# Optimization experiments

Hardware: AMD Instinct MI355X
Metric: run time of the kernel (lower is better)

Reference implementation:

```python
import jax, jax.numpy as jnp
import numpy as np

IN_FEATURES = 4096
TOKENS = 8192


def setup_inputs() -> dict:
    key = jax.random.key(0)
    k1, k2, k3 = jax.random.split(key, 3)
    x = jax.random.normal(k1, (TOKENS, IN_FEATURES), dtype=jnp.float32)
    # original init: uniform(-1, 1)
    weight = jax.random.uniform(k2, (IN_FEATURES,), dtype=jnp.float32, minval=-1.0, maxval=1.0)
    bias = jax.random.uniform(k3, (IN_FEATURES,), dtype=jnp.float32, minval=-1.0, maxval=1.0)
    return {"x": x, "weight": weight, "bias": bias}


def reference(x, weight, bias):
    # F.linear(x, eye(n) * w) + b == x * w + b (elementwise over last dim)
    return x * weight + bias
```

## Files before the change

### kernel.cpp

```cpp
#include <hip/hip_runtime.h>


#define IN_FEATURES 4096
#define VEC 4
#define WVECS (IN_FEATURES / VEC)

__global__ __launch_bounds__(256) void one_to_one_kernel(
        const float4* __restrict__ x,
        const float4* __restrict__ w,
        const float4* __restrict__ b,
        float4* __restrict__ out,
        int nvec) {
    int i = blockIdx.x * blockDim.x + threadIdx.x;
    if (i >= nvec) return;

    int col = i & (WVECS - 1);

    float4 xv = x[i];
    float4 wv = w[col];
    float4 bv = b[col];
    float4 ov;
    ov.x = fmaf(xv.x, wv.x, bv.x);
    ov.y = fmaf(xv.y, wv.y, bv.y);
    ov.z = fmaf(xv.z, wv.z, bv.z);
    ov.w = fmaf(xv.w, wv.w, bv.w);
    out[i] = ov;
}

extern "C" void kernel_launch(void* const* d_in, const int* in_sizes, int n_in,
                              void* d_out, int out_size, void* d_ws, size_t ws_size,
                              hipStream_t stream) {
    const float4* x = (const float4*)d_in[0];
    const float4* w = (const float4*)d_in[1];
    const float4* b = (const float4*)d_in[2];
    float4* out = (float4*)d_out;

    int nvec = out_size / VEC;
    int block = 256;
    int grid = (nvec + block - 1) / block;

    one_to_one_kernel<<<grid, block, 0, stream>>>(x, w, b, out, nvec);
}
```

Baseline: 223.0 us.

## Use grid-stride loop with unrolled nontemporal loads/stores and hoisted weight/bias

Replaces the one-thread-per-vector launch with a fixed 2048-block grid-stride loop. Because the stride is a multiple of the row width, each thread loads weight and bias once and keeps them in registers. The loop issues four nontemporal loads before computing, and writes with nontemporal stores so the streamed data does not pollute the cache. It adds loop overhead and, with a fixed grid, risks leaving fewer waves in flight to hide memory latency.

```diff
diff --git a/kernel.cpp b/kernel.cpp
--- a/kernel.cpp
+++ b/kernel.cpp
@@ -5,39 +5,60 @@
 #define VEC 4
 #define WVECS (IN_FEATURES / VEC)
 
-__global__ __launch_bounds__(256) void one_to_one_kernel(
-        const float4* __restrict__ x,
-        const float4* __restrict__ w,
-        const float4* __restrict__ b,
-        float4* __restrict__ out,
+#define BLOCK 256
+#define GRID 2048
+#define UNROLL 4
+
+typedef float f32x4 __attribute__((ext_vector_type(4)));
+
+__global__ __launch_bounds__(BLOCK) void one_to_one_kernel(
+        const f32x4* __restrict__ x,
+        const f32x4* __restrict__ w,
+        const f32x4* __restrict__ b,
+        f32x4* __restrict__ out,
         int nvec) {
-    int i = blockIdx.x * blockDim.x + threadIdx.x;
-    if (i >= nvec) return;
+    const int tid    = blockIdx.x * BLOCK + (int)threadIdx.x;
+    const int stride = GRID * BLOCK;
 
-    int col = i & (WVECS - 1);
+    const int col = tid & (WVECS - 1);
+    const f32x4 wv = w[col];
+    const f32x4 bv = b[col];
 
-    float4 xv = x[i];
-    float4 wv = w[col];
-    float4 bv = b[col];
-    float4 ov;
-    ov.x = fmaf(xv.x, wv.x, bv.x);
-    ov.y = fmaf(xv.y, wv.y, bv.y);
-    ov.z = fmaf(xv.z, wv.z, bv.z);
-    ov.w = fmaf(xv.w, wv.w, bv.w);
-    out[i] = ov;
+    int i = tid;
+    for (; i + (UNROLL - 1) * stride < nvec; i += UNROLL * stride) {
+        f32x4 xv[UNROLL];
+#pragma unroll
+        for (int u = 0; u < UNROLL; ++u)
+            xv[u] = __builtin_nontemporal_load(&x[i + u * stride]);
+#pragma unroll
+        for (int u = 0; u < UNROLL; ++u) {
+            f32x4 ov;
+            ov.x = fmaf(xv[u].x, wv.x, bv.x);
+            ov.y = fmaf(xv[u].y, wv.y, bv.y);
+            ov.z = fmaf(xv[u].z, wv.z, bv.z);
+            ov.w = fmaf(xv[u].w, wv.w, bv.w);
+            __builtin_nontemporal_store(ov, &out[i + u * stride]);
+        }
+    }
+    for (; i < nvec; i += stride) {
+        f32x4 xv = __builtin_nontemporal_load(&x[i]);
+        f32x4 ov;
+        ov.x = fmaf(xv.x, wv.x, bv.x);
+        ov.y = fmaf(xv.y, wv.y, bv.y);
+        ov.z = fmaf(xv.z, wv.z, bv.z);
+        ov.w = fmaf(xv.w, wv.w, bv.w);
+        __builtin_nontemporal_store(ov, &out[i]);
+    }
 }
 
 extern "C" void kernel_launch(void* const* d_in, const int* in_sizes, int n_in,
                               void* d_out, int out_size, void* d_ws, size_t ws_size,
                               hipStream_t stream) {
-    const float4* x = (const float4*)d_in[0];
-    const float4* w = (const float4*)d_in[1];
-    const float4* b = (const float4*)d_in[2];
-    float4* out = (float4*)d_out;
+    const f32x4* x = (const f32x4*)d_in[0];
+    const f32x4* w = (const f32x4*)d_in[1];
+    const f32x4* b = (const f32x4*)d_in[2];
+    f32x4* out = (f32x4*)d_out;
 
     int nvec = out_size / VEC;
-    int block = 256;
-    int grid = (nvec + block - 1) / block;
-
-    one_to_one_kernel<<<grid, block, 0, stream>>>(x, w, b, out, nvec);
+    one_to_one_kernel<<<GRID, BLOCK, 0, stream>>>(x, w, b, out, nvec);
 }
```

Measured after the change: 230.5 us. 3.4% more time.
